# Optimization experiments

Hardware: AMD Instinct MI355X
Metric: run time of the kernel (lower is better)

The kernel has to match this reference:

```python
import jax, jax.numpy as jnp
import numpy as np

N = 8192
F_IN = 1024
F_OUT = 256
ALPHA = 0.2          # LeakyReLU negative slope
ADJ_DENSITY = 0.004  # pre-symmetrization edge probability -> avg degree ~65
NEG_INF = -9.0e15    # matches -9000000000000000.0 in the torch code


def setup_inputs() -> dict:
    key = jax.random.key(0)
    k_h, k_W, k_a, k_adj = jax.random.split(key, 4)
    h = jax.random.normal(k_h, (N, F_IN), dtype=jnp.float32)
    # xavier_uniform with gain=1.414
    lim_W = 1.414 * np.sqrt(6.0 / (F_IN + F_OUT))
    W = jax.random.uniform(k_W, (F_IN, F_OUT), dtype=jnp.float32, minval=-lim_W, maxval=lim_W)
    lim_a = 1.414 * np.sqrt(6.0 / (2 * F_OUT + 1))
    a = jax.random.uniform(k_a, (2 * F_OUT, 1), dtype=jnp.float32, minval=-lim_a, maxval=lim_a)
    # sparse symmetric 0/1 adjacency (float, like the torch code's dense adj)
    u = jax.random.uniform(k_adj, (N, N))
    m = u < ADJ_DENSITY
    adj = (m | m.T).astype(jnp.float32)
    return {"h": h, "adj": adj, "W": W, "a": a}


def reference(h, adj, W, a):
    # --- GAT attention ---
    Wh = h @ W                                   # [N, F_OUT]
    Wh1 = Wh @ a[:F_OUT]                          # [N, 1]
    Wh2 = Wh @ a[F_OUT:]                          # [N, 1]
    e = jax.nn.leaky_relu(Wh1 + Wh2.T, negative_slope=ALPHA)   # [N, N]
    attention = jax.nn.softmax(jnp.where(adj > 0, e, NEG_INF), axis=1)

    # --- per-row variable-k pruning of attention + attention@attention.T ---
    n = adj.shape[0]
    diag = jnp.eye(n, dtype=bool)
    adj_nodiag = jnp.where(diag, 0.0, adj)
    s2 = jnp.count_nonzero(adj_nodiag, axis=1)    # [N] int, variable k per row

    attention2step = attention @ attention.T      # [N, N] dense GEMM
    comb = attention + attention2step
    comb = jnp.where(diag, 0.0, comb)

    # threshold = s2[i]-th largest value of row i (np.partition(row, -k)[-k])
    sorted_desc = -jnp.sort(-comb, axis=1)        # [N, N] descending per row
    idx = jnp.maximum(s2 - 1, 0)[:, None]         # clamp for s2==0 rows
    thr = jnp.take_along_axis(sorted_desc, idx, axis=1)   # [N, 1]
    # keep values >= threshold (torch code zeros values strictly < partition);
    # rows with s2 == 0 are zeroed entirely
    pruned = jnp.where((s2[:, None] > 0) & (comb >= thr), comb, 0.0)
    adj_resize = (pruned > 0).astype(jnp.float32)

    # --- output (eval mode: dropout is identity); concat=True -> ELU ---
    h_prime = attention @ Wh                      # [N, F_OUT]
    return jax.nn.elu(h_prime), adj_resize
```

## Files before the change

### kernel.cpp

```cpp
#include <hip/hip_runtime.h>
#include <cstdint>
#include <cstddef>

#define NN 8192
#define KFIN 1024
#define KFOUT 256
#define MAXD 192
#define LRALPHA 0.2f

typedef float f32x4 __attribute__((ext_vector_type(4)));

__global__ void __launch_bounds__(256) k_build_csr(
    const float* __restrict__ adj, int* __restrict__ nbr,
    int* __restrict__ deg, int* __restrict__ s2v) {
  const int wave = threadIdx.x >> 6;
  const int lane = threadIdx.x & 63;
  const int row = blockIdx.x * 4 + wave;
  const float* arow = adj + (size_t)row * NN;
  int* outp = nbr + (size_t)row * MAXD;
  int count = 0;
  int dflag = 0;
  const unsigned long long below = (1ull << lane) - 1ull;
  for (int c0 = 0; c0 < NN; c0 += 256) {
    const int c = c0 + lane * 4;
    const f32x4 v = __builtin_nontemporal_load(
        reinterpret_cast<const f32x4*>(arow + c));
    const unsigned long long m0 = __ballot(v[0] > 0.0f);
    const unsigned long long m1 = __ballot(v[1] > 0.0f);
    const unsigned long long m2 = __ballot(v[2] > 0.0f);
    const unsigned long long m3 = __ballot(v[3] > 0.0f);
    int pos = count + (int)(__popcll(m0 & below) + __popcll(m1 & below) +
                            __popcll(m2 & below) + __popcll(m3 & below));
    if (v[0] > 0.0f) { if (pos < MAXD) outp[pos] = c + 0; ++pos; if (c + 0 == row) dflag = 1; }
    if (v[1] > 0.0f) { if (pos < MAXD) outp[pos] = c + 1; ++pos; if (c + 1 == row) dflag = 1; }
    if (v[2] > 0.0f) { if (pos < MAXD) outp[pos] = c + 2; ++pos; if (c + 2 == row) dflag = 1; }
    if (v[3] > 0.0f) { if (pos < MAXD) outp[pos] = c + 3; ++pos; if (c + 3 == row) dflag = 1; }
    count += (int)(__popcll(m0) + __popcll(m1) + __popcll(m2) + __popcll(m3));
  }
  const int anyd = __any(dflag) ? 1 : 0;
  if (lane == 0) {
    deg[row] = count < MAXD ? count : MAXD;
    s2v[row] = count - anyd;
  }
}

__global__ void __launch_bounds__(256) k_gemm(
    const float* __restrict__ A, const float* __restrict__ B,
    float* __restrict__ C) {
  __shared__ float As[16][65];
  __shared__ float Bs[16][65];
  const int tid = threadIdx.x;
  const int brow = blockIdx.y * 64;
  const int bcol = blockIdx.x * 64;
  const int tx = tid & 15;
  const int ty = tid >> 4;
  float acc[4][4];
#pragma unroll
  for (int i = 0; i < 4; ++i)
#pragma unroll
    for (int j = 0; j < 4; ++j) acc[i][j] = 0.0f;
  const int ar = tid >> 2;
  const int ac = (tid & 3) << 2;
  const int br = tid >> 4;
  const int bc = (tid & 15) << 2;
  for (int k0 = 0; k0 < KFIN; k0 += 16) {
    const float4 av =
        *reinterpret_cast<const float4*>(A + (size_t)(brow + ar) * KFIN + k0 + ac);
    const float4 bv =
        *reinterpret_cast<const float4*>(B + (size_t)(k0 + br) * KFOUT + bcol + bc);
    As[ac + 0][ar] = av.x;
    As[ac + 1][ar] = av.y;
    As[ac + 2][ar] = av.z;
    As[ac + 3][ar] = av.w;
    Bs[br][bc + 0] = bv.x;
    Bs[br][bc + 1] = bv.y;
    Bs[br][bc + 2] = bv.z;
    Bs[br][bc + 3] = bv.w;
    __syncthreads();
#pragma unroll
    for (int kk = 0; kk < 16; ++kk) {
      const float a0 = As[kk][ty * 4 + 0];
      const float a1 = As[kk][ty * 4 + 1];
      const float a2 = As[kk][ty * 4 + 2];
      const float a3 = As[kk][ty * 4 + 3];
      const float b0 = Bs[kk][tx * 4 + 0];
      const float b1 = Bs[kk][tx * 4 + 1];
      const float b2 = Bs[kk][tx * 4 + 2];
      const float b3 = Bs[kk][tx * 4 + 3];
      acc[0][0] += a0 * b0; acc[0][1] += a0 * b1; acc[0][2] += a0 * b2; acc[0][3] += a0 * b3;
      acc[1][0] += a1 * b0; acc[1][1] += a1 * b1; acc[1][2] += a1 * b2; acc[1][3] += a1 * b3;
      acc[2][0] += a2 * b0; acc[2][1] += a2 * b1; acc[2][2] += a2 * b2; acc[2][3] += a2 * b3;
      acc[3][0] += a3 * b0; acc[3][1] += a3 * b1; acc[3][2] += a3 * b2; acc[3][3] += a3 * b3;
    }
    __syncthreads();
  }
#pragma unroll
  for (int i = 0; i < 4; ++i) {
#pragma unroll
    for (int j = 0; j < 4; ++j) {
      C[(size_t)(brow + ty * 4 + i) * KFOUT + bcol + tx * 4 + j] = acc[i][j];
    }
  }
}

__global__ void __launch_bounds__(256) k_rowdots(
    const float* __restrict__ Wh, const float* __restrict__ a,
    float* __restrict__ Wh1, float* __restrict__ Wh2) {
  __shared__ float sA[256];
  __shared__ float sB[256];
  const int row = blockIdx.x;
  const int t = threadIdx.x;
  const float w = Wh[(size_t)row * KFOUT + t];
  sA[t] = w * a[t];
  sB[t] = w * a[KFOUT + t];
  __syncthreads();
  for (int s = 128; s > 0; s >>= 1) {
    if (t < s) {
      sA[t] += sA[t + s];
      sB[t] += sB[t + s];
    }
    __syncthreads();
  }
  if (t == 0) {
    Wh1[row] = sA[0];
    Wh2[row] = sB[0];
  }
}

__global__ void __launch_bounds__(256) k_stats(
    const int* __restrict__ nbr, const int* __restrict__ deg,
    const float* __restrict__ Wh1, const float* __restrict__ Wh2,
    float* __restrict__ mrow, float* __restrict__ Zrow) {
  const int wave = threadIdx.x >> 6;
  const int lane = threadIdx.x & 63;
  const int row = blockIdx.x * 4 + wave;
  const int d = deg[row];
  const int* cols = nbr + (size_t)row * MAXD;
  const float w1 = Wh1[row];
  float mx = -1e30f;
  for (int t = lane; t < d; t += 64) {
    float e = w1 + Wh2[cols[t]];
    e = e > 0.0f ? e : LRALPHA * e;
    mx = fmaxf(mx, e);
  }
  for (int o = 32; o > 0; o >>= 1) mx = fmaxf(mx, __shfl_xor(mx, o));
  float sum = 0.0f;
  for (int t = lane; t < d; t += 64) {
    float e = w1 + Wh2[cols[t]];
    e = e > 0.0f ? e : LRALPHA * e;
    sum += expf(e - mx);
  }
  for (int o = 32; o > 0; o >>= 1) sum += __shfl_xor(sum, o);
  if (lane == 0) {
    mrow[row] = mx;
    Zrow[row] = (d > 0) ? sum : 1.0f;
  }
}

__global__ void __launch_bounds__(256) k_att(
    const int* __restrict__ nbr, const int* __restrict__ deg,
    const float* __restrict__ Wh1, const float* __restrict__ Wh2,
    const float* __restrict__ mrow, const float* __restrict__ Zrow,
    float* __restrict__ att, int2* __restrict__ edgesT,
    short4* __restrict__ qb) {
  const int wave = threadIdx.x >> 6;
  const int lane = threadIdx.x & 63;
  const int row = blockIdx.x * 4 + wave;
  const int d = deg[row];
  const int* cols = nbr + (size_t)row * MAXD;
  const float w1r = Wh1[row];
  const float w2r = Wh2[row];
  const float mr = mrow[row];
  const float invZr = 1.0f / Zrow[row];
  int b1 = 0, b2 = 0, b3 = 0;
  for (int t0 = 0; t0 < d; t0 += 64) {
    const int t = t0 + lane;
    const bool act = t < d;
    const int j = act ? cols[t] : 0x7fffffff;
    b1 += (int)__popcll(__ballot(act && j < 2048));
    b2 += (int)__popcll(__ballot(act && j < 4096));
    b3 += (int)__popcll(__ballot(act && j < 6144));
    if (act) {
      float e = w1r + Wh2[j];
      e = e > 0.0f ? e : LRALPHA * e;
      att[(size_t)row * MAXD + t] = expf(e - mr) * invZr;
      float e2 = Wh1[j] + w2r;
      e2 = e2 > 0.0f ? e2 : LRALPHA * e2;
      const float v = expf(e2 - mrow[j]) / Zrow[j];
      edgesT[(size_t)row * MAXD + t] = make_int2(j, __float_as_int(v));
    }
  }
  if (lane == 0) {
    qb[row] = make_short4((short)b1, (short)b2, (short)b3, (short)d);
  }
}

__global__ void __launch_bounds__(256) k_twostep(
    const int* __restrict__ nbr, const int* __restrict__ deg,
    const int* __restrict__ s2v, const float* __restrict__ att,
    const int2* __restrict__ edgesT, const short4* __restrict__ qbg,
    float* __restrict__ out1) {
  __shared__ float comb[NN];
  __shared__ float wvals[MAXD];
  __shared__ int kcols[MAXD];
  __shared__ short sqb[MAXD][4];
  __shared__ unsigned int hist[256];
  __shared__ unsigned int shPrefix;
  __shared__ int shRemaining;
  const int tid = threadIdx.x;
  const int wave = tid >> 6;
  const int lane = tid & 63;
  const int row = blockIdx.x;
  const f32x4 z4 = {0.0f, 0.0f, 0.0f, 0.0f};
  for (int j = tid * 4; j < NN; j += 1024)
    *reinterpret_cast<f32x4*>(&comb[j]) = z4;
  const int d = deg[row];
  const int* cols = nbr + (size_t)row * MAXD;
  const float* arow = att + (size_t)row * MAXD;
  for (int t = tid; t < d; t += 256) {
    const int c = cols[t];
    kcols[t] = c;
    wvals[t] = arow[t];
    *reinterpret_cast<short4*>(&sqb[t][0]) = qbg[c];
  }
  __syncthreads();
  const int clo = wave << 11;
  const int chi = clo + 2048;
  {
    int2 a_e = make_int2(0, 0), b_e = make_int2(0, 0);
    int a_qs = 0, a_qe = 0, b_qs = 0, b_qe = 0;
    float a_w = 0.0f, b_w = 0.0f;
    const int2 *a_ek = edgesT, *b_ek = edgesT;
#define ISSUE_SLOT(E_, QS_, QE_, W_, EK_, KI)                          \
    {                                                                   \
      const int k_ = kcols[KI];                                         \
      W_ = wvals[KI];                                                   \
      QS_ = (wave == 0) ? 0 : (int)sqb[KI][wave - 1];                   \
      QE_ = (int)sqb[KI][wave];                                         \
      EK_ = edgesT + (size_t)k_ * MAXD;                                 \
      E_ = make_int2(0, 0);                                             \
      if (lane < QE_ - QS_) E_ = EK_[QS_ + lane];                       \
    }
    if (d > 0) ISSUE_SLOT(a_e, a_qs, a_qe, a_w, a_ek, 0);
    if (d > 1) ISSUE_SLOT(b_e, b_qs, b_qe, b_w, b_ek, 1);
    for (int kidx = 0; kidx < d; ++kidx) {
      const int2 e = a_e;
      const int qs = a_qs, qe = a_qe;
      const float w = a_w;
      const int2* ek = a_ek;
      a_e = b_e; a_qs = b_qs; a_qe = b_qe; a_w = b_w; a_ek = b_ek;
      if (kidx + 2 < d) ISSUE_SLOT(b_e, b_qs, b_qe, b_w, b_ek, kidx + 2);
      if (lane < qe - qs) comb[e.x] += w * __int_as_float(e.y);
      for (int t = qs + 64 + lane; t < qe; t += 64) {
        const int2 e2 = ek[t];
        comb[e2.x] += w * __int_as_float(e2.y);
      }
    }
#undef ISSUE_SLOT
  }
  for (int t = lane; t < d; t += 64) {
    const int c = kcols[t];
    if (c >= clo && c < chi) comb[c] += wvals[t];
  }
  __syncthreads();
  if (tid == 0) comb[row] = 0.0f;
  __syncthreads();
  const int kk = s2v[row];
  const size_t obase = (size_t)row * NN;
  if (kk <= 0) {
    for (int j = tid * 4; j < NN; j += 1024)
      __builtin_nontemporal_store(z4, reinterpret_cast<f32x4*>(&out1[obase + j]));
    return;
  }
  unsigned int prefix = 0u;
  int remaining = kk;
  for (int pass = 0; pass < 4; ++pass) {
    const int shift = 24 - 8 * pass;
    const unsigned int pmask = (pass == 0) ? 0u : (0xFFFFFFFFu << (shift + 8));
    hist[tid] = 0u;
    __syncthreads();
    for (int j = tid; j < NN; j += 256) {
      const unsigned int u = __float_as_uint(comb[j]);
      if (u != 0u && (u & pmask) == prefix)
        atomicAdd(&hist[(u >> shift) & 255u], 1u);
    }
    __syncthreads();
    if (tid < 64) {
      const int bHi = 255 - 4 * lane;
      const unsigned int c0 = hist[bHi];
      const unsigned int c1 = hist[bHi - 1];
      const unsigned int c2 = hist[bHi - 2];
      const unsigned int c3 = hist[bHi - 3];
      const unsigned int gs = c0 + c1 + c2 + c3;
      unsigned int run = gs;
      for (int o = 1; o < 64; o <<= 1) {
        const unsigned int tt = __shfl_up(run, o);
        if (lane >= o) run += tt;
      }
      const unsigned int pre = run - gs;
      const unsigned int rem = (unsigned int)remaining;
      if (pre < rem && pre + gs >= rem) {
        unsigned int above;
        int digit;
        if (pre + c0 >= rem) { digit = bHi; above = pre; }
        else if (pre + c0 + c1 >= rem) { digit = bHi - 1; above = pre + c0; }
        else if (pre + c0 + c1 + c2 >= rem) { digit = bHi - 2; above = pre + c0 + c1; }
        else { digit = bHi - 3; above = pre + c0 + c1 + c2; }
        shPrefix = prefix | ((unsigned int)digit << shift);
        shRemaining = remaining - (int)above;
      }
    }
    __syncthreads();
    prefix = shPrefix;
    remaining = shRemaining;
    __syncthreads();
  }
  const float thr = __uint_as_float(prefix);
  for (int j = tid * 4; j < NN; j += 1024) {
    const f32x4 cv = *reinterpret_cast<const f32x4*>(&comb[j]);
    f32x4 ov;
    ov[0] = (cv[0] >= thr && cv[0] > 0.0f) ? 1.0f : 0.0f;
    ov[1] = (cv[1] >= thr && cv[1] > 0.0f) ? 1.0f : 0.0f;
    ov[2] = (cv[2] >= thr && cv[2] > 0.0f) ? 1.0f : 0.0f;
    ov[3] = (cv[3] >= thr && cv[3] > 0.0f) ? 1.0f : 0.0f;
    __builtin_nontemporal_store(ov, reinterpret_cast<f32x4*>(&out1[obase + j]));
  }
}

__global__ void __launch_bounds__(256) k_hprime(
    const int* __restrict__ nbr, const int* __restrict__ deg,
    const float* __restrict__ att, const float* __restrict__ Wh,
    float* __restrict__ out0) {
  __shared__ int scol[MAXD];
  __shared__ float sval[MAXD];
  const int row = blockIdx.x;
  const int c = threadIdx.x;
  const int d = deg[row];
  const int* cols = nbr + (size_t)row * MAXD;
  const float* arow = att + (size_t)row * MAXD;
  for (int t = threadIdx.x; t < d; t += 256) {
    scol[t] = cols[t];
    sval[t] = arow[t];
  }
  __syncthreads();
  float a0 = 0.0f, a1 = 0.0f, a2 = 0.0f, a3 = 0.0f;
  int t = 0;
  for (; t + 4 <= d; t += 4) {
    a0 += sval[t + 0] * Wh[(size_t)scol[t + 0] * KFOUT + c];
    a1 += sval[t + 1] * Wh[(size_t)scol[t + 1] * KFOUT + c];
    a2 += sval[t + 2] * Wh[(size_t)scol[t + 2] * KFOUT + c];
    a3 += sval[t + 3] * Wh[(size_t)scol[t + 3] * KFOUT + c];
  }
  for (; t < d; ++t) a0 += sval[t] * Wh[(size_t)scol[t] * KFOUT + c];
  const float acc = (a0 + a1) + (a2 + a3);
  out0[(size_t)row * KFOUT + c] = acc > 0.0f ? acc : expm1f(acc);
}

extern "C" void kernel_launch(void* const* d_in, const int* in_sizes, int n_in,
                              void* d_out, int out_size, void* d_ws, size_t ws_size,
                              hipStream_t stream) {
  const float* h = (const float*)d_in[0];
  const float* adj = (const float*)d_in[1];
  const float* W = (const float*)d_in[2];
  const float* a = (const float*)d_in[3];

  float* out0 = (float*)d_out;
  float* out1 = out0 + (size_t)NN * KFOUT;

  float* Wh = (float*)d_ws;
  float* Wh1 = Wh + (size_t)NN * KFOUT;
  float* Wh2 = Wh1 + NN;
  float* mrow = Wh2 + NN;
  float* Zrow = mrow + NN;
  float* att = Zrow + NN;
  float* edgesF = att + (size_t)NN * MAXD;
  int2* edgesT = (int2*)edgesF;
  int* nbr = (int*)(edgesF + (size_t)NN * MAXD * 2);
  int* deg = nbr + (size_t)NN * MAXD;
  int* s2v = deg + NN;
  short4* qb = (short4*)(s2v + NN);

  k_build_csr<<<NN / 4, 256, 0, stream>>>(adj, nbr, deg, s2v);
  dim3 ggrid(KFOUT / 64, NN / 64);
  k_gemm<<<ggrid, 256, 0, stream>>>(h, W, Wh);
  k_rowdots<<<NN, 256, 0, stream>>>(Wh, a, Wh1, Wh2);
  k_stats<<<NN / 4, 256, 0, stream>>>(nbr, deg, Wh1, Wh2, mrow, Zrow);
  k_att<<<NN / 4, 256, 0, stream>>>(nbr, deg, Wh1, Wh2, mrow, Zrow, att, edgesT, qb);
  k_twostep<<<NN, 256, 0, stream>>>(nbr, deg, s2v, att, edgesT, qb, out1);
  k_hprime<<<NN, 256, 0, stream>>>(nbr, deg, att, Wh, out0);
}
```

Baseline: 517.1 us.

## Flatten two-step edge scatter with prefix-sum load balancing across eight column waves

k_twostep now uses 512 threads, and the column range is split into eight 1024-wide bands, one per wave. k_att records seven split counts per neighbour list. Each wave builds a prefix sum of its per-neighbour edge counts, then processes a flat stream of edges 64 at a time, using binary search to find the owning neighbour. Contributions go in through LDS atomicAdd. This replaces per-neighbour loops in which lanes sat idle when a neighbour had few edges in the band. The histogram pass also reads comb with vector loads. The trade-offs are binary-search overhead, LDS atomics, and more shared memory for the prefix arrays.

```diff
diff --git a/kernel.cpp b/kernel.cpp
--- a/kernel.cpp
+++ b/kernel.cpp
@@ -162,7 +162,7 @@
     const float* __restrict__ Wh1, const float* __restrict__ Wh2,
     const float* __restrict__ mrow, const float* __restrict__ Zrow,
     float* __restrict__ att, int2* __restrict__ edgesT,
-    short4* __restrict__ qb) {
+    short* __restrict__ qb8) {
   const int wave = threadIdx.x >> 6;
   const int lane = threadIdx.x & 63;
   const int row = blockIdx.x * 4 + wave;
@@ -172,14 +172,14 @@
   const float w2r = Wh2[row];
   const float mr = mrow[row];
   const float invZr = 1.0f / Zrow[row];
-  int b1 = 0, b2 = 0, b3 = 0;
+  int b[7] = {0, 0, 0, 0, 0, 0, 0};
   for (int t0 = 0; t0 < d; t0 += 64) {
     const int t = t0 + lane;
     const bool act = t < d;
     const int j = act ? cols[t] : 0x7fffffff;
-    b1 += (int)__popcll(__ballot(act && j < 2048));
-    b2 += (int)__popcll(__ballot(act && j < 4096));
-    b3 += (int)__popcll(__ballot(act && j < 6144));
+#pragma unroll
+    for (int m = 1; m <= 7; ++m)
+      b[m - 1] += (int)__popcll(__ballot(act && j < m * 1024));
     if (act) {
       float e = w1r + Wh2[j];
       e = e > 0.0f ? e : LRALPHA * e;
@@ -191,19 +191,22 @@
     }
   }
   if (lane == 0) {
-    qb[row] = make_short4((short)b1, (short)b2, (short)b3, (short)d);
-  }
-}
-
-__global__ void __launch_bounds__(256) k_twostep(
+    short* q = qb8 + (size_t)row * 8;
+    q[0] = (short)b[0]; q[1] = (short)b[1]; q[2] = (short)b[2]; q[3] = (short)b[3];
+    q[4] = (short)b[4]; q[5] = (short)b[5]; q[6] = (short)b[6]; q[7] = (short)d;
+  }
+}
+
+__global__ void __launch_bounds__(512) k_twostep(
     const int* __restrict__ nbr, const int* __restrict__ deg,
     const int* __restrict__ s2v, const float* __restrict__ att,
-    const int2* __restrict__ edgesT, const short4* __restrict__ qbg,
+    const int2* __restrict__ edgesT, const short* __restrict__ qb8,
     float* __restrict__ out1) {
   __shared__ float comb[NN];
   __shared__ float wvals[MAXD];
   __shared__ int kcols[MAXD];
-  __shared__ short sqb[MAXD][4];
+  __shared__ short sqb[MAXD][8];
+  __shared__ int pfx[8][MAXD + 1];
   __shared__ unsigned int hist[256];
   __shared__ unsigned int shPrefix;
   __shared__ int shRemaining;
@@ -212,55 +215,74 @@
   const int lane = tid & 63;
   const int row = blockIdx.x;
   const f32x4 z4 = {0.0f, 0.0f, 0.0f, 0.0f};
-  for (int j = tid * 4; j < NN; j += 1024)
+  for (int j = tid * 4; j < NN; j += 2048)
     *reinterpret_cast<f32x4*>(&comb[j]) = z4;
   const int d = deg[row];
   const int* cols = nbr + (size_t)row * MAXD;
   const float* arow = att + (size_t)row * MAXD;
-  for (int t = tid; t < d; t += 256) {
+  for (int t = tid; t < d; t += 512) {
     const int c = cols[t];
     kcols[t] = c;
     wvals[t] = arow[t];
-    *reinterpret_cast<short4*>(&sqb[t][0]) = qbg[c];
+    *reinterpret_cast<int4*>(&sqb[t][0]) =
+        *reinterpret_cast<const int4*>(&qb8[(size_t)c * 8]);
   }
   __syncthreads();
-  const int clo = wave << 11;
-  const int chi = clo + 2048;
+  int run = 0;
+  for (int t0 = 0; t0 < d; t0 += 64) {
+    const int t = t0 + lane;
+    int len = 0;
+    if (t < d) {
+      const int lo = wave ? (int)sqb[t][wave - 1] : 0;
+      len = (int)sqb[t][wave] - lo;
+    }
+    int scan = len;
+#pragma unroll
+    for (int o = 1; o < 64; o <<= 1) {
+      const int v = __shfl_up(scan, o);
+      if (lane >= o) scan += v;
+    }
+    if (t < d) pfx[wave][t + 1] = run + scan;
+    run += __shfl(scan, 63);
+  }
+  if (lane == 0) pfx[wave][0] = 0;
+  const int Ew = run;
   {
-    int2 a_e = make_int2(0, 0), b_e = make_int2(0, 0);
-    int a_qs = 0, a_qe = 0, b_qs = 0, b_qe = 0;
-    float a_w = 0.0f, b_w = 0.0f;
-    const int2 *a_ek = edgesT, *b_ek = edgesT;
-#define ISSUE_SLOT(E_, QS_, QE_, W_, EK_, KI)                          \
-    {                                                                   \
-      const int k_ = kcols[KI];                                         \
-      W_ = wvals[KI];                                                   \
-      QS_ = (wave == 0) ? 0 : (int)sqb[KI][wave - 1];                   \
-      QE_ = (int)sqb[KI][wave];                                         \
-      EK_ = edgesT + (size_t)k_ * MAXD;                                 \
-      E_ = make_int2(0, 0);                                             \
-      if (lane < QE_ - QS_) E_ = EK_[QS_ + lane];                       \
-    }
-    if (d > 0) ISSUE_SLOT(a_e, a_qs, a_qe, a_w, a_ek, 0);
-    if (d > 1) ISSUE_SLOT(b_e, b_qs, b_qe, b_w, b_ek, 1);
-    for (int kidx = 0; kidx < d; ++kidx) {
-      const int2 e = a_e;
-      const int qs = a_qs, qe = a_qe;
-      const float w = a_w;
-      const int2* ek = a_ek;
-      a_e = b_e; a_qs = b_qs; a_qe = b_qe; a_w = b_w; a_ek = b_ek;
-      if (kidx + 2 < d) ISSUE_SLOT(b_e, b_qs, b_qe, b_w, b_ek, kidx + 2);
-      if (lane < qe - qs) comb[e.x] += w * __int_as_float(e.y);
-      for (int t = qs + 64 + lane; t < qe; t += 64) {
-        const int2 e2 = ek[t];
-        comb[e2.x] += w * __int_as_float(e2.y);
-      }
-    }
-#undef ISSUE_SLOT
-  }
-  for (int t = lane; t < d; t += 64) {
-    const int c = kcols[t];
-    if (c >= clo && c < chi) comb[c] += wvals[t];
+    const int* pw = pfx[wave];
+    int2 eA = make_int2(0, 0), eB = make_int2(0, 0);
+    float wA = 0.0f, wB = 0.0f;
+    bool aA = false, aB = false;
+#define TS_ISSUE(E_, W_, A_, BASE)                                    \
+    {                                                                  \
+      const int eidx = (BASE) + lane;                                  \
+      A_ = eidx < Ew;                                                  \
+      const int ei = A_ ? eidx : 0;                                    \
+      int lo = 0, hi = d - 1;                                          \
+      while (lo < hi) {                                                \
+        const int mid = (lo + hi + 1) >> 1;                            \
+        if (pw[mid] <= ei) lo = mid; else hi = mid - 1;                \
+      }                                                                \
+      const int off = ei - pw[lo];                                     \
+      const int qs = wave ? (int)sqb[lo][wave - 1] : 0;                \
+      W_ = wvals[lo];                                                  \
+      E_ = make_int2(0, 0);                                            \
+      if (A_) E_ = edgesT[(size_t)kcols[lo] * MAXD + qs + off];        \
+    }
+    if (Ew > 0) TS_ISSUE(eA, wA, aA, 0);
+    if (Ew > 64) TS_ISSUE(eB, wB, aB, 64);
+    for (int base = 0; base < Ew; base += 64) {
+      const int2 e = eA; const float w = wA; const bool a = aA;
+      eA = eB; wA = wB; aA = aB;
+      if (base + 128 < Ew) TS_ISSUE(eB, wB, aB, base + 128);
+      if (a) atomicAdd(&comb[e.x], w * __int_as_float(e.y));
+    }
+#undef TS_ISSUE
+  }
+  {
+    const short* qr = qb8 + (size_t)row * 8;
+    const int qlo = wave ? (int)qr[wave - 1] : 0;
+    const int qhi = (int)qr[wave];
+    for (int t = qlo + lane; t < qhi; t += 64) comb[kcols[t]] += wvals[t];
   }
   __syncthreads();
   if (tid == 0) comb[row] = 0.0f;
@@ -268,7 +290,7 @@
   const int kk = s2v[row];
   const size_t obase = (size_t)row * NN;
   if (kk <= 0) {
-    for (int j = tid * 4; j < NN; j += 1024)
+    for (int j = tid * 4; j < NN; j += 2048)
       __builtin_nontemporal_store(z4, reinterpret_cast<f32x4*>(&out1[obase + j]));
     return;
   }
@@ -277,12 +299,16 @@
   for (int pass = 0; pass < 4; ++pass) {
     const int shift = 24 - 8 * pass;
     const unsigned int pmask = (pass == 0) ? 0u : (0xFFFFFFFFu << (shift + 8));
-    hist[tid] = 0u;
-    __syncthreads();
-    for (int j = tid; j < NN; j += 256) {
-      const unsigned int u = __float_as_uint(comb[j]);
-      if (u != 0u && (u & pmask) == prefix)
-        atomicAdd(&hist[(u >> shift) & 255u], 1u);
+    if (tid < 256) hist[tid] = 0u;
+    __syncthreads();
+    for (int j = tid * 4; j < NN; j += 2048) {
+      const f32x4 cv = *reinterpret_cast<const f32x4*>(&comb[j]);
+#pragma unroll
+      for (int q = 0; q < 4; ++q) {
+        const unsigned int u = __float_as_uint(cv[q]);
+        if (u != 0u && (u & pmask) == prefix)
+          atomicAdd(&hist[(u >> shift) & 255u], 1u);
+      }
     }
     __syncthreads();
     if (tid < 64) {
@@ -292,12 +318,12 @@
       const unsigned int c2 = hist[bHi - 2];
       const unsigned int c3 = hist[bHi - 3];
       const unsigned int gs = c0 + c1 + c2 + c3;
-      unsigned int run = gs;
+      unsigned int run2 = gs;
       for (int o = 1; o < 64; o <<= 1) {
-        const unsigned int tt = __shfl_up(run, o);
-        if (lane >= o) run += tt;
+        const unsigned int tt = __shfl_up(run2, o);
+        if (lane >= o) run2 += tt;
       }
-      const unsigned int pre = run - gs;
+      const unsigned int pre = run2 - gs;
       const unsigned int rem = (unsigned int)remaining;
       if (pre < rem && pre + gs >= rem) {
         unsigned int above;
@@ -316,7 +342,7 @@
     __syncthreads();
   }
   const float thr = __uint_as_float(prefix);
-  for (int j = tid * 4; j < NN; j += 1024) {
+  for (int j = tid * 4; j < NN; j += 2048) {
     const f32x4 cv = *reinterpret_cast<const f32x4*>(&comb[j]);
     f32x4 ov;
     ov[0] = (cv[0] >= thr && cv[0] > 0.0f) ? 1.0f : 0.0f;
@@ -378,14 +404,14 @@
   int* nbr = (int*)(edgesF + (size_t)NN * MAXD * 2);
   int* deg = nbr + (size_t)NN * MAXD;
   int* s2v = deg + NN;
-  short4* qb = (short4*)(s2v + NN);
+  short* qb8 = (short*)(s2v + NN);
 
   k_build_csr<<<NN / 4, 256, 0, stream>>>(adj, nbr, deg, s2v);
   dim3 ggrid(KFOUT / 64, NN / 64);
   k_gemm<<<ggrid, 256, 0, stream>>>(h, W, Wh);
   k_rowdots<<<NN, 256, 0, stream>>>(Wh, a, Wh1, Wh2);
   k_stats<<<NN / 4, 256, 0, stream>>>(nbr, deg, Wh1, Wh2, mrow, Zrow);
-  k_att<<<NN / 4, 256, 0, stream>>>(nbr, deg, Wh1, Wh2, mrow, Zrow, att, edgesT, qb);
-  k_twostep<<<NN, 256, 0, stream>>>(nbr, deg, s2v, att, edgesT, qb, out1);
+  k_att<<<NN / 4, 256, 0, stream>>>(nbr, deg, Wh1, Wh2, mrow, Zrow, att, edgesT, qb8);
+  k_twostep<<<NN, 512, 0, stream>>>(nbr, deg, s2v, att, edgesT, qb8, out1);
   k_hprime<<<NN, 256, 0, stream>>>(nbr, deg, att, Wh, out0);
 }
```

Measured after the change: 558.9 us. +8.1%, slower.
